# Performance work log

Hardware: AMD Instinct MI355X
Metric: run time of the kernel (lower is better)

The kernel has to match this reference:

```python
import jax, jax.numpy as jnp
import numpy as np

B, Z, H, W, C = 8, 16, 32, 32, 512
C8 = C // 8
N = Z * H * W
EPS = 1e-3  # Keras BatchNormalization default epsilon


def setup_inputs() -> dict:
    key = jax.random.key(0)
    ks = jax.random.split(key, 8)
    scale = 0.05
    x = jax.random.normal(ks[0], (B, Z, H, W, C), jnp.float32)
    return {
        "x": x,
        "bn1_gamma": jnp.ones((C,), jnp.float32),
        "bn1_beta": jnp.zeros((C,), jnp.float32),
        "bn1_mean": jax.random.normal(ks[1], (C,), jnp.float32) * 0.1,
        "bn1_var": jnp.abs(jax.random.normal(ks[2], (C,), jnp.float32)) * 0.1 + 1.0,
        "wq": jax.random.normal(ks[3], (C, C8), jnp.float32) * scale,
        "bq": jnp.zeros((C8,), jnp.float32),
        "wk": jax.random.normal(ks[4], (C, C8), jnp.float32) * scale,
        "bk": jnp.zeros((C8,), jnp.float32),
        "wv": jax.random.normal(ks[5], (C, C8), jnp.float32) * scale,
        "bv": jnp.zeros((C8,), jnp.float32),
        "wp": jax.random.normal(ks[6], (C8, C), jnp.float32) * scale,
        "bp": jnp.zeros((C,), jnp.float32),
        "bn2_gamma": jnp.ones((C,), jnp.float32),
        "bn2_beta": jnp.zeros((C,), jnp.float32),
        "bn2_mean": jax.random.normal(ks[7], (C,), jnp.float32) * 0.1,
        "bn2_var": jnp.ones((C,), jnp.float32),
    }


def _bn(t, gamma, beta, mean, var):
    # Keras BatchNormalization (inference), channels-last axis=-1
    return (t - mean) * jax.lax.rsqrt(var + EPS) * gamma + beta


def _conv1x1(t, w, b):
    # 1x1x1 Conv3D == per-voxel channel matmul
    return jnp.einsum('bzhwc,cd->bzhwd', t, w) + b


def reference(x, bn1_gamma, bn1_beta, bn1_mean, bn1_var,
              wq, bq, wk, bk, wv, bv, wp, bp,
              bn2_gamma, bn2_beta, bn2_mean, bn2_var):
    img = _bn(x, bn1_gamma, bn1_beta, bn1_mean, bn1_var)
    q = _conv1x1(img, wq, bq).reshape(B, N, C8)  # (B, N, c)
    k = _conv1x1(img, wk, bk).reshape(B, N, C8)  # (B, N, c)
    v = _conv1x1(img, wv, bv).reshape(B, N, C8)  # (B, N, c)
    # Keras Dot(axes=[1,2])([q, permute(k)]): contracts the N axis of both
    # -> channel Gram matrix s[b,i,j] = sum_n q[b,n,i] * k[b,n,j]
    s = jnp.einsum('bni,bnj->bij', q, k)          # (B, c, c)
    beta = jax.nn.softmax(s, axis=-1)             # (B, c, c)
    # Keras Dot(axes=[1,2])([beta, v]): attn[b,i,j] = sum_m beta[b,m,i] * v[b,j,m]
    attn = jnp.einsum('bmi,bjm->bij', beta, v)    # (B, c, N)
    # Keras Reshape((Z,H,W,c)) on (B, c, N): row-major reinterpretation
    out = attn.reshape(B, Z, H, W, C8)
    out = _conv1x1(out, wp, bp)                   # (B, Z, H, W, C)
    out = _bn(out, bn2_gamma, bn2_beta, bn2_mean, bn2_var)
    return out
```

## Files before the change

### kernel.cpp

```cpp
#include <hip/hip_runtime.h>

#define EPS 1e-3f

typedef _Float16 f16;
typedef _Float16 f16x8 __attribute__((ext_vector_type(8)));
typedef _Float16 f16x4 __attribute__((ext_vector_type(4)));
typedef float f32x4 __attribute__((ext_vector_type(4)));

constexpr int Bn = 8, C = 512, C8 = 64;
constexpr int N = 16384;
constexpr int M = Bn * N;

constexpr size_t OFF_WHI  = 0;
constexpr size_t OFF_WLO  = 196608;
constexpr size_t OFF_BQKV = 327680;
constexpr size_t OFF_WPT  = 328704;
constexpr size_t OFF_BOUT = 394240;
constexpr size_t OFF_QK   = 396288;
constexpr size_t OFF_V    = OFF_QK + (size_t)M * 128 * 2;
constexpr size_t OFF_PART = OFF_V + (size_t)M * 64 * 2;
constexpr size_t OFF_BT   = OFF_PART + (size_t)8*16*4096*4;

__global__ __launch_bounds__(256) void k0_fold(
    const float* g1, const float* be1, const float* mu1, const float* va1,
    const float* wq, const float* bq, const float* wk, const float* bk,
    const float* wv, const float* bv, const float* wp, const float* bp,
    const float* g2, const float* be2, const float* mu2, const float* va2,
    char* ws)
{
  f16* whi = (f16*)(ws + OFF_WHI);
  f16* wlo = (f16*)(ws + OFF_WLO);
  float* bqkv = (float*)(ws + OFF_BQKV);
  f16* wpt = (f16*)(ws + OFF_WPT);
  float* bout = (float*)(ws + OFF_BOUT);
  __shared__ float red[256];
  int blk = blockIdx.x, t = threadIdx.x;
  if (blk < 192) {
    const float* w; const float* bb; int col;
    if (blk < 64)       { w = wq; bb = bq; col = blk; }
    else if (blk < 128) { w = wk; bb = bk; col = blk - 64; }
    else                { w = wv; bb = bv; col = blk - 128; }
    float part = 0.f;
    for (int c = t; c < 512; c += 256) {
      float a1 = g1[c] * rsqrtf(va1[c] + EPS);
      float d1 = be1[c] - mu1[c] * a1;
      float wval = w[c * 64 + col];
      float fw = a1 * wval;
      f16 hi = (f16)fw;
      whi[blk * 512 + c] = hi;
      if (blk < 128) wlo[blk * 512 + c] = (f16)((fw - (float)hi) * 2048.0f);
      part += d1 * wval;
    }
    red[t] = part; __syncthreads();
    for (int s = 128; s > 0; s >>= 1) { if (t < s) red[t] += red[t + s]; __syncthreads(); }
    if (t == 0) bqkv[blk] = red[0] + bb[col];
  } else {
    int co = blk - 192;
    float a2 = g2[co] * rsqrtf(va2[co] + EPS);
    if (t < 64) wpt[co * 64 + t] = (f16)(wp[t * 512 + co] * a2);
    if (t == 0) bout[co] = (bp[co] - mu2[co]) * a2 + be2[co];
  }
}

__global__ __launch_bounds__(256, 2) void k1_qkv(const float* __restrict__ x, char* __restrict__ ws)
{
  const f16* whi = (const f16*)(ws + OFF_WHI);
  const f16* wlo = (const f16*)(ws + OFF_WLO);
  const float* bqkv = (const float*)(ws + OFF_BQKV);
  f16* qkbuf = (f16*)(ws + OFF_QK);
  f16* vbuf  = (f16*)(ws + OFF_V);

  __shared__ f16 xs[64 * 40];

  int t = threadIdx.x;
  int wave = t >> 6, lane = t & 63;
  int m0 = blockIdx.x * 64;

  int nt0 = wave, nt1 = wave + 4, nt2 = wave + 8;

  f32x4 acc_h[4][2], acc_l[4][2], acc_v[4];
  for (int i = 0; i < 4; i++) {
    for (int j = 0; j < 2; j++) { acc_h[i][j] = (f32x4){0.f,0.f,0.f,0.f}; acc_l[i][j] = (f32x4){0.f,0.f,0.f,0.f}; }
    acc_v[i] = (f32x4){0.f,0.f,0.f,0.f};
  }

  int arow = t >> 3;
  int acol = (t & 7) * 4;
  const float* xg = x + (size_t)(m0 + arow) * 512 + acol;

  int bn0 = nt0 * 16 + (lane & 15);
  int bn1 = nt1 * 16 + (lane & 15);
  int bn2 = nt2 * 16 + (lane & 15);
  int bko = (lane >> 4) * 8;

  f32x4 a0 = *(const f32x4*)(xg);
  f32x4 a1 = *(const f32x4*)(xg + 32 * 512);
  f16x8 b0h = *(const f16x8*)(whi + bn0 * 512 + bko);
  f16x8 b1h = *(const f16x8*)(whi + bn1 * 512 + bko);
  f16x8 b2h = *(const f16x8*)(whi + bn2 * 512 + bko);
  f16x8 b0l = *(const f16x8*)(wlo + bn0 * 512 + bko);
  f16x8 b1l = *(const f16x8*)(wlo + bn1 * 512 + bko);

  for (int kc = 0; kc < 16; kc++) {
    f16x4 h0, h1;
    for (int e = 0; e < 4; e++) { h0[e] = (f16)a0[e]; h1[e] = (f16)a1[e]; }
    *(f16x4*)&xs[arow * 40 + acol] = h0;
    *(f16x4*)&xs[(arow + 32) * 40 + acol] = h1;
    __syncthreads();

    f16x8 B0h = b0h, B1h = b1h, B2h = b2h, B0l = b0l, B1l = b1l;
    if (kc < 15) {
      const float* xg2 = xg + (kc + 1) * 32;
      a0 = *(const f32x4*)(xg2);
      a1 = *(const f32x4*)(xg2 + 32 * 512);
      int ko = (kc + 1) * 32 + bko;
      b0h = *(const f16x8*)(whi + bn0 * 512 + ko);
      b1h = *(const f16x8*)(whi + bn1 * 512 + ko);
      b2h = *(const f16x8*)(whi + bn2 * 512 + ko);
      b0l = *(const f16x8*)(wlo + bn0 * 512 + ko);
      b1l = *(const f16x8*)(wlo + bn1 * 512 + ko);
    }

    int aoff = (lane & 15) * 40 + (lane >> 4) * 8;
    for (int mt = 0; mt < 4; mt++) {
      f16x8 af = *(const f16x8*)&xs[mt * 16 * 40 + aoff];
      acc_h[mt][0] = __builtin_amdgcn_mfma_f32_16x16x32_f16(af, B0h, acc_h[mt][0], 0, 0, 0);
      acc_h[mt][1] = __builtin_amdgcn_mfma_f32_16x16x32_f16(af, B1h, acc_h[mt][1], 0, 0, 0);
      acc_l[mt][0] = __builtin_amdgcn_mfma_f32_16x16x32_f16(af, B0l, acc_l[mt][0], 0, 0, 0);
      acc_l[mt][1] = __builtin_amdgcn_mfma_f32_16x16x32_f16(af, B1l, acc_l[mt][1], 0, 0, 0);
      acc_v[mt]    = __builtin_amdgcn_mfma_f32_16x16x32_f16(af, B2h, acc_v[mt],    0, 0, 0);
    }
    __syncthreads();
  }

  const float inv2048 = 1.0f / 2048.0f;
  int colA = nt0 * 16 + (lane & 15);
  int colB = nt1 * 16 + (lane & 15);
  int colV = nt2 * 16 + (lane & 15);
  float bA = bqkv[colA], bB = bqkv[colB], bV = bqkv[colV];
  int rbase = m0 + (lane >> 4) * 4;
  for (int mt = 0; mt < 4; mt++) {
    for (int r = 0; r < 4; r++) {
      size_t row = (size_t)(rbase + mt * 16 + r);
      qkbuf[row * 128 + colA] = (f16)(acc_h[mt][0][r] + acc_l[mt][0][r] * inv2048 + bA);
      qkbuf[row * 128 + colB] = (f16)(acc_h[mt][1][r] + acc_l[mt][1][r] * inv2048 + bB);
      vbuf[row * 64 + (colV - 128)] = (f16)(acc_v[mt][r] + bV);
    }
  }
}

__global__ __launch_bounds__(256) void k2a_gram(char* __restrict__ ws)
{
  const f16* qkbuf = (const f16*)(ws + OFF_QK);
  float* part = (float*)(ws + OFF_PART);
  __shared__ f16 tlds[128 * 40];
  int t = threadIdx.x, wave = t >> 6, lane = t & 63;
  int b = blockIdx.x >> 4, ch = blockIdx.x & 15;
  size_t base = (size_t)(b * 16384 + ch * 1024) * 128;

  f32x4 acc[4];
  for (int i = 0; i < 4; i++) acc[i] = (f32x4){0.f,0.f,0.f,0.f};

  int lrow = t >> 3;
  int lcol = (t & 7) * 16;

  for (int it = 0; it < 32; it++) {
    const f16* src = qkbuf + base + (size_t)(it * 32 + lrow) * 128 + lcol;
    f16x8 v0 = *(const f16x8*)(src);
    f16x8 v1 = *(const f16x8*)(src + 8);
    __syncthreads();
    for (int e = 0; e < 8; e++) tlds[(lcol + e) * 40 + lrow] = v0[e];
    for (int e = 0; e < 8; e++) tlds[(lcol + 8 + e) * 40 + lrow] = v1[e];
    __syncthreads();
    int koff = (lane >> 4) * 8;
    f16x8 bf = *(const f16x8*)&tlds[(64 + wave * 16 + (lane & 15)) * 40 + koff];
    for (int itile = 0; itile < 4; itile++) {
      f16x8 af = *(const f16x8*)&tlds[(itile * 16 + (lane & 15)) * 40 + koff];
      acc[itile] = __builtin_amdgcn_mfma_f32_16x16x32_f16(af, bf, acc[itile], 0, 0, 0);
    }
  }
  float* dst = part + (size_t)blockIdx.x * 4096;
  int j = wave * 16 + (lane & 15);
  for (int itile = 0; itile < 4; itile++)
    for (int r = 0; r < 4; r++) {
      int i = itile * 16 + (lane >> 4) * 4 + r;
      dst[i * 64 + j] = acc[itile][r];
    }
}

__global__ __launch_bounds__(256) void k2b_softmax(char* __restrict__ ws)
{
  const float* part = (const float*)(ws + OFF_PART);
  f16* bt = (f16*)(ws + OFF_BT);
  __shared__ float s[4096];
  int b = blockIdx.x, t = threadIdx.x;
  for (int cell = t; cell < 4096; cell += 256) {
    float sum = 0.f;
    for (int ch = 0; ch < 16; ch++) sum += part[(size_t)(b * 16 + ch) * 4096 + cell];
    s[cell] = sum;
  }
  __syncthreads();
  if (t < 64) {
    float mx = -1e30f;
    for (int j = 0; j < 64; j++) mx = fmaxf(mx, s[t * 64 + j]);
    float e[64]; float den = 0.f;
    for (int j = 0; j < 64; j++) { e[j] = __expf(s[t * 64 + j] - mx); den += e[j]; }
    float inv = 1.0f / den;
    for (int j = 0; j < 64; j++) bt[(size_t)b * 4096 + j * 64 + t] = (f16)(e[j] * inv);
  }
}

__global__ __launch_bounds__(256) void k3_attn(char* __restrict__ ws)
{
  const f16* vbuf = (const f16*)(ws + OFF_V);
  const f16* bt = (const f16*)(ws + OFF_BT);
  f16* attn = (f16*)(ws + OFF_QK);
  int t = threadIdx.x, wave = t >> 6, lane = t & 63;
  int b = blockIdx.x >> 6, jc = blockIdx.x & 63;
  int j0 = jc * 256 + wave * 64;

  f32x4 acc[4][4];
  for (int i = 0; i < 4; i++) for (int j = 0; j < 4; j++) acc[i][j] = (f32x4){0.f,0.f,0.f,0.f};

  int koff = (lane >> 4) * 8;
  for (int km = 0; km < 2; km++) {
    f16x8 af[4], bf[4];
    for (int it = 0; it < 4; it++)
      af[it] = *(const f16x8*)(bt + (size_t)b * 4096 + (it * 16 + (lane & 15)) * 64 + km * 32 + koff);
    for (int jt = 0; jt < 4; jt++)
      bf[jt] = *(const f16x8*)(vbuf + (size_t)(b * 16384 + j0 + jt * 16 + (lane & 15)) * 64 + km * 32 + koff);
    for (int it = 0; it < 4; it++)
      for (int jt = 0; jt < 4; jt++)
        acc[it][jt] = __builtin_amdgcn_mfma_f32_16x16x32_f16(af[it], bf[jt], acc[it][jt], 0, 0, 0);
  }
  size_t abase = (size_t)b * 1048576;
  for (int it = 0; it < 4; it++)
    for (int jt = 0; jt < 4; jt++)
      for (int r = 0; r < 4; r++) {
        int i = it * 16 + (lane >> 4) * 4 + r;
        int j = j0 + jt * 16 + (lane & 15);
        attn[abase + (size_t)i * 16384 + j] = (f16)acc[it][jt][r];
      }
}

__global__ __launch_bounds__(256, 2) void k4_proj(const char* __restrict__ ws, float* __restrict__ out)
{
  const f16* attn = (const f16*)(ws + OFF_QK);
  const f16* wpt = (const f16*)(ws + OFF_WPT);
  const float* bout = (const float*)(ws + OFF_BOUT);
  int t = threadIdx.x, wave = t >> 6, lane = t & 63;
  int m0 = blockIdx.x * 64;
  int c0 = wave * 128;

  f32x4 acc[4][8];
  for (int i = 0; i < 4; i++) for (int j = 0; j < 8; j++) acc[i][j] = (f32x4){0.f,0.f,0.f,0.f};
  int koff = (lane >> 4) * 8;
  for (int km = 0; km < 2; km++) {
    f16x8 af[4], bf[8];
    for (int mt = 0; mt < 4; mt++)
      af[mt] = *(const f16x8*)(attn + (size_t)(m0 + mt * 16 + (lane & 15)) * 64 + km * 32 + koff);
    for (int nt = 0; nt < 8; nt++)
      bf[nt] = *(const f16x8*)(wpt + (size_t)(c0 + nt * 16 + (lane & 15)) * 64 + km * 32 + koff);
    for (int mt = 0; mt < 4; mt++)
      for (int nt = 0; nt < 8; nt++)
        acc[mt][nt] = __builtin_amdgcn_mfma_f32_16x16x32_f16(af[mt], bf[nt], acc[mt][nt], 0, 0, 0);
  }
  for (int nt = 0; nt < 8; nt++) {
    int c = c0 + nt * 16 + (lane & 15);
    float bc = bout[c];
    for (int mt = 0; mt < 4; mt++)
      for (int r = 0; r < 4; r++) {
        int row = m0 + mt * 16 + (lane >> 4) * 4 + r;
        out[(size_t)row * 512 + c] = acc[mt][nt][r] + bc;
      }
  }
}

extern "C" void kernel_launch(void* const* d_in, const int* in_sizes, int n_in,
                              void* d_out, int out_size, void* d_ws, size_t ws_size,
                              hipStream_t stream)
{
  const float* x   = (const float*)d_in[0];
  const float* g1  = (const float*)d_in[1];
  const float* be1 = (const float*)d_in[2];
  const float* mu1 = (const float*)d_in[3];
  const float* va1 = (const float*)d_in[4];
  const float* wq  = (const float*)d_in[5];
  const float* bq  = (const float*)d_in[6];
  const float* wk  = (const float*)d_in[7];
  const float* bk  = (const float*)d_in[8];
  const float* wv  = (const float*)d_in[9];
  const float* bv  = (const float*)d_in[10];
  const float* wp  = (const float*)d_in[11];
  const float* bp  = (const float*)d_in[12];
  const float* g2  = (const float*)d_in[13];
  const float* be2 = (const float*)d_in[14];
  const float* mu2 = (const float*)d_in[15];
  const float* va2 = (const float*)d_in[16];
  char* ws = (char*)d_ws;
  float* out = (float*)d_out;

  k0_fold<<<dim3(704), dim3(256), 0, stream>>>(g1, be1, mu1, va1, wq, bq, wk, bk,
                                               wv, bv, wp, bp, g2, be2, mu2, va2, ws);
  k1_qkv<<<dim3(2048), dim3(256), 0, stream>>>(x, ws);
  k2a_gram<<<dim3(128), dim3(256), 0, stream>>>(ws);
  k2b_softmax<<<dim3(8), dim3(256), 0, stream>>>(ws);
  k3_attn<<<dim3(512), dim3(256), 0, stream>>>(ws);
  k4_proj<<<dim3(2048), dim3(256), 0, stream>>>(ws, out);
}
```

Measured before the change: 590.6 us.

## Fuse attention and projection kernels, atomic Gram reduction, restructure QKV tiling

Result: faster. 578.9 us (-2.0%).

```diff
diff --git a/kernel.cpp b/kernel.cpp
--- a/kernel.cpp
+++ b/kernel.cpp
@@ -18,8 +18,8 @@
 constexpr size_t OFF_BOUT = 394240;
 constexpr size_t OFF_QK   = 396288;
 constexpr size_t OFF_V    = OFF_QK + (size_t)M * 128 * 2;
-constexpr size_t OFF_PART = OFF_V + (size_t)M * 64 * 2;
-constexpr size_t OFF_BT   = OFF_PART + (size_t)8*16*4096*4;
+constexpr size_t OFF_S    = OFF_V + (size_t)M * 64 * 2;
+constexpr size_t OFF_BT   = OFF_S + (size_t)8 * 4096 * 4;
 
 __global__ __launch_bounds__(256) void k0_fold(
     const float* g1, const float* be1, const float* mu1, const float* va1,
@@ -33,6 +33,7 @@
   float* bqkv = (float*)(ws + OFF_BQKV);
   f16* wpt = (f16*)(ws + OFF_WPT);
   float* bout = (float*)(ws + OFF_BOUT);
+  float* sbuf = (float*)(ws + OFF_S);
   __shared__ float red[256];
   int blk = blockIdx.x, t = threadIdx.x;
   if (blk < 192) {
@@ -59,6 +60,7 @@
     float a2 = g2[co] * rsqrtf(va2[co] + EPS);
     if (t < 64) wpt[co * 64 + t] = (f16)(wp[t * 512 + co] * a2);
     if (t == 0) bout[co] = (bp[co] - mu2[co]) * a2 + be2[co];
+    if (t < 64) sbuf[co * 64 + t] = 0.0f;
   }
 }
 
@@ -70,13 +72,19 @@
   f16* qkbuf = (f16*)(ws + OFF_QK);
   f16* vbuf  = (f16*)(ws + OFF_V);
 
-  __shared__ f16 xs[64 * 40];
+  __shared__ f16 xs[2][64 * 72];
 
   int t = threadIdx.x;
   int wave = t >> 6, lane = t & 63;
   int m0 = blockIdx.x * 64;
 
-  int nt0 = wave, nt1 = wave + 4, nt2 = wave + 8;
+  int srow = t >> 2, scol = (t & 3) * 4;
+  const float* xg = x + (size_t)(m0 + srow) * 512 + scol;
+
+  int bn0 = wave * 16 + (lane & 15);
+  int bn1 = bn0 + 64;
+  int bn2 = bn0 + 128;
+  int klane = (lane >> 4) * 8;
 
   f32x4 acc_h[4][2], acc_l[4][2], acc_v[4];
   for (int i = 0; i < 4; i++) {
@@ -84,195 +92,189 @@
     acc_v[i] = (f32x4){0.f,0.f,0.f,0.f};
   }
 
-  int arow = t >> 3;
-  int acol = (t & 7) * 4;
-  const float* xg = x + (size_t)(m0 + arow) * 512 + acol;
-
-  int bn0 = nt0 * 16 + (lane & 15);
-  int bn1 = nt1 * 16 + (lane & 15);
-  int bn2 = nt2 * 16 + (lane & 15);
-  int bko = (lane >> 4) * 8;
-
   f32x4 a0 = *(const f32x4*)(xg);
-  f32x4 a1 = *(const f32x4*)(xg + 32 * 512);
-  f16x8 b0h = *(const f16x8*)(whi + bn0 * 512 + bko);
-  f16x8 b1h = *(const f16x8*)(whi + bn1 * 512 + bko);
-  f16x8 b2h = *(const f16x8*)(whi + bn2 * 512 + bko);
-  f16x8 b0l = *(const f16x8*)(wlo + bn0 * 512 + bko);
-  f16x8 b1l = *(const f16x8*)(wlo + bn1 * 512 + bko);
-
-  for (int kc = 0; kc < 16; kc++) {
-    f16x4 h0, h1;
-    for (int e = 0; e < 4; e++) { h0[e] = (f16)a0[e]; h1[e] = (f16)a1[e]; }
-    *(f16x4*)&xs[arow * 40 + acol] = h0;
-    *(f16x4*)&xs[(arow + 32) * 40 + acol] = h1;
+  f32x4 a1 = *(const f32x4*)(xg + 16);
+  f32x4 a2 = *(const f32x4*)(xg + 32);
+  f32x4 a3 = *(const f32x4*)(xg + 48);
+
+  for (int iter = 0; iter < 8; iter++) {
+    f16* xb = &xs[iter & 1][0];
+    {
+      f16x4 h0, h1, h2, h3;
+      for (int e = 0; e < 4; e++) { h0[e]=(f16)a0[e]; h1[e]=(f16)a1[e]; h2[e]=(f16)a2[e]; h3[e]=(f16)a3[e]; }
+      *(f16x4*)&xb[srow * 72 + scol     ] = h0;
+      *(f16x4*)&xb[srow * 72 + scol + 16] = h1;
+      *(f16x4*)&xb[srow * 72 + scol + 32] = h2;
+      *(f16x4*)&xb[srow * 72 + scol + 48] = h3;
+    }
     __syncthreads();
-
-    f16x8 B0h = b0h, B1h = b1h, B2h = b2h, B0l = b0l, B1l = b1l;
-    if (kc < 15) {
-      const float* xg2 = xg + (kc + 1) * 32;
-      a0 = *(const f32x4*)(xg2);
-      a1 = *(const f32x4*)(xg2 + 32 * 512);
-      int ko = (kc + 1) * 32 + bko;
-      b0h = *(const f16x8*)(whi + bn0 * 512 + ko);
-      b1h = *(const f16x8*)(whi + bn1 * 512 + ko);
-      b2h = *(const f16x8*)(whi + bn2 * 512 + ko);
-      b0l = *(const f16x8*)(wlo + bn0 * 512 + ko);
-      b1l = *(const f16x8*)(wlo + bn1 * 512 + ko);
-    }
-
-    int aoff = (lane & 15) * 40 + (lane >> 4) * 8;
-    for (int mt = 0; mt < 4; mt++) {
-      f16x8 af = *(const f16x8*)&xs[mt * 16 * 40 + aoff];
-      acc_h[mt][0] = __builtin_amdgcn_mfma_f32_16x16x32_f16(af, B0h, acc_h[mt][0], 0, 0, 0);
-      acc_h[mt][1] = __builtin_amdgcn_mfma_f32_16x16x32_f16(af, B1h, acc_h[mt][1], 0, 0, 0);
-      acc_l[mt][0] = __builtin_amdgcn_mfma_f32_16x16x32_f16(af, B0l, acc_l[mt][0], 0, 0, 0);
-      acc_l[mt][1] = __builtin_amdgcn_mfma_f32_16x16x32_f16(af, B1l, acc_l[mt][1], 0, 0, 0);
-      acc_v[mt]    = __builtin_amdgcn_mfma_f32_16x16x32_f16(af, B2h, acc_v[mt],    0, 0, 0);
-    }
-    __syncthreads();
+    if (iter < 7) {
+      const float* xi = xg + (iter + 1) * 64;
+      a0 = *(const f32x4*)(xi);
+      a1 = *(const f32x4*)(xi + 16);
+      a2 = *(const f32x4*)(xi + 32);
+      a3 = *(const f32x4*)(xi + 48);
+    }
+    for (int ks = 0; ks < 2; ks++) {
+      int kg = iter * 64 + ks * 32 + klane;
+      f16x8 b0h = *(const f16x8*)(whi + bn0 * 512 + kg);
+      f16x8 b1h = *(const f16x8*)(whi + bn1 * 512 + kg);
+      f16x8 b2h = *(const f16x8*)(whi + bn2 * 512 + kg);
+      f16x8 b0l = *(const f16x8*)(wlo + bn0 * 512 + kg);
+      f16x8 b1l = *(const f16x8*)(wlo + bn1 * 512 + kg);
+      int aoff = (lane & 15) * 72 + ks * 32 + klane;
+      for (int mt = 0; mt < 4; mt++) {
+        f16x8 af = *(const f16x8*)&xb[mt * 16 * 72 + aoff];
+        acc_h[mt][0] = __builtin_amdgcn_mfma_f32_16x16x32_f16(af, b0h, acc_h[mt][0], 0, 0, 0);
+        acc_h[mt][1] = __builtin_amdgcn_mfma_f32_16x16x32_f16(af, b1h, acc_h[mt][1], 0, 0, 0);
+        acc_l[mt][0] = __builtin_amdgcn_mfma_f32_16x16x32_f16(af, b0l, acc_l[mt][0], 0, 0, 0);
+        acc_l[mt][1] = __builtin_amdgcn_mfma_f32_16x16x32_f16(af, b1l, acc_l[mt][1], 0, 0, 0);
+        acc_v[mt]    = __builtin_amdgcn_mfma_f32_16x16x32_f16(af, b2h, acc_v[mt],    0, 0, 0);
+      }
+    }
   }
 
   const float inv2048 = 1.0f / 2048.0f;
-  int colA = nt0 * 16 + (lane & 15);
-  int colB = nt1 * 16 + (lane & 15);
-  int colV = nt2 * 16 + (lane & 15);
-  float bA = bqkv[colA], bB = bqkv[colB], bV = bqkv[colV];
+  int colA = bn0, colB = bn1, colV = bn0;
+  float bA = bqkv[colA], bB = bqkv[colB], bV = bqkv[bn2];
   int rbase = m0 + (lane >> 4) * 4;
   for (int mt = 0; mt < 4; mt++) {
     for (int r = 0; r < 4; r++) {
       size_t row = (size_t)(rbase + mt * 16 + r);
       qkbuf[row * 128 + colA] = (f16)(acc_h[mt][0][r] + acc_l[mt][0][r] * inv2048 + bA);
       qkbuf[row * 128 + colB] = (f16)(acc_h[mt][1][r] + acc_l[mt][1][r] * inv2048 + bB);
-      vbuf[row * 64 + (colV - 128)] = (f16)(acc_v[mt][r] + bV);
+      vbuf[row * 64 + colV]   = (f16)(acc_v[mt][r] + bV);
     }
   }
 }
 
 __global__ __launch_bounds__(256) void k2a_gram(char* __restrict__ ws)
 {
-  const f16* qkbuf = (const f16*)(ws + OFF_QK);
-  float* part = (float*)(ws + OFF_PART);
-  __shared__ f16 tlds[128 * 40];
+  const f16* qk = (const f16*)(ws + OFF_QK);
+  float* sbuf = (float*)(ws + OFF_S);
   int t = threadIdx.x, wave = t >> 6, lane = t & 63;
-  int b = blockIdx.x >> 4, ch = blockIdx.x & 15;
-  size_t base = (size_t)(b * 16384 + ch * 1024) * 128;
+  int b = blockIdx.x >> 6, ch = blockIdx.x & 63;
+  int n0 = b * 16384 + ch * 256;
 
   f32x4 acc[4];
   for (int i = 0; i < 4; i++) acc[i] = (f32x4){0.f,0.f,0.f,0.f};
 
-  int lrow = t >> 3;
-  int lcol = (t & 7) * 16;
-
-  for (int it = 0; it < 32; it++) {
-    const f16* src = qkbuf + base + (size_t)(it * 32 + lrow) * 128 + lcol;
-    f16x8 v0 = *(const f16x8*)(src);
-    f16x8 v1 = *(const f16x8*)(src + 8);
-    __syncthreads();
-    for (int e = 0; e < 8; e++) tlds[(lcol + e) * 40 + lrow] = v0[e];
-    for (int e = 0; e < 8; e++) tlds[(lcol + 8 + e) * 40 + lrow] = v1[e];
-    __syncthreads();
-    int koff = (lane >> 4) * 8;
-    f16x8 bf = *(const f16x8*)&tlds[(64 + wave * 16 + (lane & 15)) * 40 + koff];
-    for (int itile = 0; itile < 4; itile++) {
-      f16x8 af = *(const f16x8*)&tlds[(itile * 16 + (lane & 15)) * 40 + koff];
-      acc[itile] = __builtin_amdgcn_mfma_f32_16x16x32_f16(af, bf, acc[itile], 0, 0, 0);
-    }
-  }
-  float* dst = part + (size_t)blockIdx.x * 4096;
-  int j = wave * 16 + (lane & 15);
+  int li = lane & 15;
+  int jc = 64 + wave * 16 + li;
+
+  for (int it = 0; it < 8; it++) {
+    const f16* p = qk + (size_t)(n0 + it * 32 + (lane >> 4) * 8) * 128;
+    f16x8 af0, af1, af2, af3, bf;
+#pragma unroll
+    for (int j = 0; j < 8; j++) {
+      const f16* pr = p + j * 128;
+      af0[j] = pr[li];
+      af1[j] = pr[16 + li];
+      af2[j] = pr[32 + li];
+      af3[j] = pr[48 + li];
+      bf[j]  = pr[jc];
+    }
+    acc[0] = __builtin_amdgcn_mfma_f32_16x16x32_f16(af0, bf, acc[0], 0, 0, 0);
+    acc[1] = __builtin_amdgcn_mfma_f32_16x16x32_f16(af1, bf, acc[1], 0, 0, 0);
+    acc[2] = __builtin_amdgcn_mfma_f32_16x16x32_f16(af2, bf, acc[2], 0, 0, 0);
+    acc[3] = __builtin_amdgcn_mfma_f32_16x16x32_f16(af3, bf, acc[3], 0, 0, 0);
+  }
+  int j = wave * 16 + li;
   for (int itile = 0; itile < 4; itile++)
     for (int r = 0; r < 4; r++) {
       int i = itile * 16 + (lane >> 4) * 4 + r;
-      dst[i * 64 + j] = acc[itile][r];
+      atomicAdd(&sbuf[(size_t)b * 4096 + i * 64 + j], acc[itile][r]);
     }
 }
 
 __global__ __launch_bounds__(256) void k2b_softmax(char* __restrict__ ws)
 {
-  const float* part = (const float*)(ws + OFF_PART);
+  const float* sbuf = (const float*)(ws + OFF_S);
   f16* bt = (f16*)(ws + OFF_BT);
-  __shared__ float s[4096];
   int b = blockIdx.x, t = threadIdx.x;
-  for (int cell = t; cell < 4096; cell += 256) {
-    float sum = 0.f;
-    for (int ch = 0; ch < 16; ch++) sum += part[(size_t)(b * 16 + ch) * 4096 + cell];
-    s[cell] = sum;
-  }
-  __syncthreads();
   if (t < 64) {
+    const float* srow = sbuf + (size_t)b * 4096 + t * 64;
     float mx = -1e30f;
-    for (int j = 0; j < 64; j++) mx = fmaxf(mx, s[t * 64 + j]);
+    for (int j = 0; j < 64; j++) mx = fmaxf(mx, srow[j]);
     float e[64]; float den = 0.f;
-    for (int j = 0; j < 64; j++) { e[j] = __expf(s[t * 64 + j] - mx); den += e[j]; }
+    for (int j = 0; j < 64; j++) { e[j] = __expf(srow[j] - mx); den += e[j]; }
     float inv = 1.0f / den;
     for (int j = 0; j < 64; j++) bt[(size_t)b * 4096 + j * 64 + t] = (f16)(e[j] * inv);
   }
 }
 
-__global__ __launch_bounds__(256) void k3_attn(char* __restrict__ ws)
+__device__ __forceinline__ int at_idx(int row, int d) {
+  int dd = (d >> 1) ^ (((row >> 3) & 3) << 3);
+  return row * 64 + dd * 2 + (d & 1);
+}
+
+__global__ __launch_bounds__(256, 2) void k34_attn_proj(char* __restrict__ ws, float* __restrict__ out)
 {
   const f16* vbuf = (const f16*)(ws + OFF_V);
   const f16* bt = (const f16*)(ws + OFF_BT);
-  f16* attn = (f16*)(ws + OFF_QK);
+  const f16* wpt = (const f16*)(ws + OFF_WPT);
+  const float* bout = (const float*)(ws + OFF_BOUT);
+  __shared__ f16 at[128 * 64];
+
   int t = threadIdx.x, wave = t >> 6, lane = t & 63;
-  int b = blockIdx.x >> 6, jc = blockIdx.x & 63;
-  int j0 = jc * 256 + wave * 64;
-
-  f32x4 acc[4][4];
-  for (int i = 0; i < 4; i++) for (int j = 0; j < 4; j++) acc[i][j] = (f32x4){0.f,0.f,0.f,0.f};
-
-  int koff = (lane >> 4) * 8;
+  int b = blockIdx.x >> 7, jc = blockIdx.x & 127;
+  int li = lane & 15;
+  int klane = (lane >> 4) * 8;
+
+  f32x4 acc[4][2];
+  for (int i = 0; i < 4; i++) for (int j = 0; j < 2; j++) acc[i][j] = (f32x4){0.f,0.f,0.f,0.f};
+
   for (int km = 0; km < 2; km++) {
-    f16x8 af[4], bf[4];
+    f16x8 af[4], bf[2];
     for (int it = 0; it < 4; it++)
-      af[it] = *(const f16x8*)(bt + (size_t)b * 4096 + (it * 16 + (lane & 15)) * 64 + km * 32 + koff);
-    for (int jt = 0; jt < 4; jt++)
-      bf[jt] = *(const f16x8*)(vbuf + (size_t)(b * 16384 + j0 + jt * 16 + (lane & 15)) * 64 + km * 32 + koff);
+      af[it] = *(const f16x8*)(bt + (size_t)b * 4096 + (it * 16 + li) * 64 + km * 32 + klane);
+    for (int jt = 0; jt < 2; jt++) {
+      int jrow = jc * 128 + wave * 32 + jt * 16 + li;
+      bf[jt] = *(const f16x8*)(vbuf + (size_t)(b * 16384 + jrow) * 64 + km * 32 + klane);
+    }
     for (int it = 0; it < 4; it++)
-      for (int jt = 0; jt < 4; jt++)
+      for (int jt = 0; jt < 2; jt++)
         acc[it][jt] = __builtin_amdgcn_mfma_f32_16x16x32_f16(af[it], bf[jt], acc[it][jt], 0, 0, 0);
   }
-  size_t abase = (size_t)b * 1048576;
   for (int it = 0; it < 4; it++)
-    for (int jt = 0; jt < 4; jt++)
+    for (int jt = 0; jt < 2; jt++)
       for (int r = 0; r < 4; r++) {
         int i = it * 16 + (lane >> 4) * 4 + r;
-        int j = j0 + jt * 16 + (lane & 15);
-        attn[abase + (size_t)i * 16384 + j] = (f16)acc[it][jt][r];
+        int d = (wave & 1) * 32 + jt * 16 + li;
+        at[at_idx(i * 2 + (wave >> 1), d)] = (f16)acc[it][jt][r];
       }
-}
-
-__global__ __launch_bounds__(256, 2) void k4_proj(const char* __restrict__ ws, float* __restrict__ out)
-{
-  const f16* attn = (const f16*)(ws + OFF_QK);
-  const f16* wpt = (const f16*)(ws + OFF_WPT);
-  const float* bout = (const float*)(ws + OFF_BOUT);
-  int t = threadIdx.x, wave = t >> 6, lane = t & 63;
-  int m0 = blockIdx.x * 64;
-  int c0 = wave * 128;
-
-  f32x4 acc[4][8];
-  for (int i = 0; i < 4; i++) for (int j = 0; j < 8; j++) acc[i][j] = (f32x4){0.f,0.f,0.f,0.f};
-  int koff = (lane >> 4) * 8;
-  for (int km = 0; km < 2; km++) {
-    f16x8 af[4], bf[8];
-    for (int mt = 0; mt < 4; mt++)
-      af[mt] = *(const f16x8*)(attn + (size_t)(m0 + mt * 16 + (lane & 15)) * 64 + km * 32 + koff);
-    for (int nt = 0; nt < 8; nt++)
-      bf[nt] = *(const f16x8*)(wpt + (size_t)(c0 + nt * 16 + (lane & 15)) * 64 + km * 32 + koff);
-    for (int mt = 0; mt < 4; mt++)
-      for (int nt = 0; nt < 8; nt++)
-        acc[mt][nt] = __builtin_amdgcn_mfma_f32_16x16x32_f16(af[mt], bf[nt], acc[mt][nt], 0, 0, 0);
-  }
-  for (int nt = 0; nt < 8; nt++) {
-    int c = c0 + nt * 16 + (lane & 15);
-    float bc = bout[c];
-    for (int mt = 0; mt < 4; mt++)
-      for (int r = 0; r < 4; r++) {
-        int row = m0 + mt * 16 + (lane >> 4) * 4 + r;
-        out[(size_t)row * 512 + c] = acc[mt][nt][r] + bc;
-      }
+  __syncthreads();
+
+  f16x8 paf[2][2];
+  for (int mt = 0; mt < 2; mt++)
+    for (int km = 0; km < 2; km++) {
+      int row = wave * 32 + mt * 16 + li;
+      int d = km * 32 + klane;
+      paf[mt][km] = *(const f16x8*)&at[row * 64 + ((((d >> 1) ^ (((row >> 3) & 3) << 3))) << 1)];
+    }
+  size_t obase = (size_t)b * 16384 * 512;
+  for (int strip = 0; strip < 8; strip++) {
+    int c0 = strip * 64;
+    f16x8 pbf[2][4];
+    for (int nt = 0; nt < 4; nt++)
+      for (int km = 0; km < 2; km++)
+        pbf[km][nt] = *(const f16x8*)(wpt + (size_t)(c0 + nt * 16 + li) * 64 + km * 32 + klane);
+    f32x4 pac[2][4];
+    for (int mt = 0; mt < 2; mt++) for (int nt = 0; nt < 4; nt++) pac[mt][nt] = (f32x4){0.f,0.f,0.f,0.f};
+    for (int km = 0; km < 2; km++)
+      for (int mt = 0; mt < 2; mt++)
+        for (int nt = 0; nt < 4; nt++)
+          pac[mt][nt] = __builtin_amdgcn_mfma_f32_16x16x32_f16(paf[mt][km], pbf[km][nt], pac[mt][nt], 0, 0, 0);
+    for (int nt = 0; nt < 4; nt++) {
+      int c = c0 + nt * 16 + li;
+      float bc = bout[c];
+      for (int mt = 0; mt < 2; mt++)
+        for (int r = 0; r < 4; r++) {
+          int rl = wave * 32 + mt * 16 + (lane >> 4) * 4 + r;
+          int pos = (rl >> 1) * 256 + jc * 2 + (rl & 1);
+          out[obase + (size_t)pos * 512 + c] = pac[mt][nt][r] + bc;
+        }
+    }
   }
 }
 
@@ -303,8 +305,7 @@
   k0_fold<<<dim3(704), dim3(256), 0, stream>>>(g1, be1, mu1, va1, wq, bq, wk, bk,
                                                wv, bv, wp, bp, g2, be2, mu2, va2, ws);
   k1_qkv<<<dim3(2048), dim3(256), 0, stream>>>(x, ws);
-  k2a_gram<<<dim3(128), dim3(256), 0, stream>>>(ws);
+  k2a_gram<<<dim3(512), dim3(256), 0, stream>>>(ws);
   k2b_softmax<<<dim3(8), dim3(256), 0, stream>>>(ws);
-  k3_attn<<<dim3(512), dim3(256), 0, stream>>>(ws);
-  k4_proj<<<dim3(2048), dim3(256), 0, stream>>>(ws, out);
-}
+  k34_attn_proj<<<dim3(1024), dim3(256), 0, stream>>>(ws, out);
+}
```
